# Kernel optimization log

Hardware: AMD Instinct MI355X
Metric: run time of the kernel (lower is better)

## Reference

```python
import jax, jax.numpy as jnp
import numpy as np

B, T, D, H, L, C = 64, 256, 128, 1024, 5, 10


def setup_inputs() -> dict:
    key = jax.random.key(0)
    ks = jax.random.split(key, 6)
    def init(k, shape, fan_in):
        return jax.random.normal(k, shape, jnp.float32) / np.float32(np.sqrt(fan_in))
    x = jax.random.normal(ks[0], (B, T, D), jnp.float32)
    Wx0 = init(ks[1], (D, 4 * H), D)            # layer 0 input weights
    Wxs = init(ks[2], (L - 1, H, 4 * H), H)     # layers 1..L-1 input weights
    Whs = init(ks[3], (L, H, 4 * H), H)         # recurrent weights
    bs = jnp.zeros((L, 4 * H), jnp.float32)     # gate biases
    W_head = init(ks[4], (H, C), H)
    b_head = jnp.zeros((C,), jnp.float32)
    return {"x": x, "Wx0": Wx0, "Wxs": Wxs, "Whs": Whs, "bs": bs,
            "W_head": W_head, "b_head": b_head}


def _lstm_layer(xs, Wx, Wh, b):
    # xs: [T, B, in_d] time-major; returns hidden sequence [T, B, H]
    Bsz = xs.shape[1]
    Hd = Wh.shape[0]
    def step(carry, x_t):
        c, h = carry
        z = x_t @ Wx + h @ Wh + b            # [B, 4H], gate order i,f,g,o (flax)
        i, f, g, o = jnp.split(z, 4, axis=-1)
        c_new = jax.nn.sigmoid(f) * c + jax.nn.sigmoid(i) * jnp.tanh(g)
        h_new = jax.nn.sigmoid(o) * jnp.tanh(c_new)
        return (c_new, h_new), h_new
    init = (jnp.zeros((Bsz, Hd), xs.dtype), jnp.zeros((Bsz, Hd), xs.dtype))
    _, hs = jax.lax.scan(step, init, xs)
    return hs


def reference(x, Wx0, Wxs, Whs, bs, W_head, b_head):
    xs = jnp.swapaxes(x, 0, 1)                  # [T, B, D]
    xs = _lstm_layer(xs, Wx0, Whs[0], bs[0])
    for l in range(1, L):
        xs = _lstm_layer(xs, Wxs[l - 1], Whs[l], bs[l])
    return xs[-1] @ W_head + b_head             # [B, C] from last timestep
```

## Files before the change

### kernel.cpp

```cpp
#include <hip/hip_runtime.h>
#include <hip/hip_cooperative_groups.h>
#include <hip/hip_bf16.h>
#include <cstddef>

namespace cg = cooperative_groups;

typedef unsigned short u16;
typedef __attribute__((ext_vector_type(8))) short s8;
typedef __attribute__((ext_vector_type(4))) float f4;

constexpr int kB = 64, kT = 256, kD = 128, kH = 1024, kL = 5, kC = 10, kG = 4096;
constexpr int BH = kB * kH;
constexpr size_t WLA_ELEMS = (size_t)256 * 8 * 16384;
constexpr size_t WLB_ELEMS = (size_t)256 * 8 * 2560;
constexpr size_t H_ELEMS = (size_t)kL * 2 * BH;


__device__ __forceinline__ float sigf(float x) { return 1.f / (1.f + __expf(-x)); }
__device__ __forceinline__ float tanh_s(float x) {
  float ax = fabsf(x);
  float e = __expf(-2.f * ax);
  float r = (1.f - e) / (1.f + e);
  return copysignf(r, x);
}
__device__ __forceinline__ void split_bf16(float v, short& hi, short& lo) {
  __hip_bfloat16 h = __float2bfloat16(v);
  hi = __builtin_bit_cast(short, h);
  float fh = __bfloat162float(h);
  __hip_bfloat16 l = __float2bfloat16(v - fh);
  lo = __builtin_bit_cast(short, l);
}
__device__ __forceinline__ short hi_bf16(float v) {
  __hip_bfloat16 h = __float2bfloat16(v);
  return __builtin_bit_cast(short, h);
}
__device__ __forceinline__ float bf2f(u16 v) {
  unsigned u = ((unsigned)v) << 16;
  return __builtin_bit_cast(float, u);
}

__device__ __forceinline__ void dma16(const void* gsrc, void* ldst) {
  __builtin_amdgcn_global_load_lds(
      (const __attribute__((address_space(1))) void*)gsrc,
      (__attribute__((address_space(3))) void*)ldst, 16, 0, 0);
}

__global__ void __launch_bounds__(512) split_wl(const float* __restrict__ Wx0,
                                                const float* __restrict__ Wxs,
                                                const float* __restrict__ Whs,
                                                u16* __restrict__ wlA,
                                                u16* __restrict__ wlB) {
  const int g = blockIdx.x, tid = threadIdx.x;
  const int wv = tid >> 6, lane = tid & 63, quad = lane >> 4, r = lane & 15;
  const int lA = (g >> 6) + 1, jb = g & 63, kq = wv & 3, ch = wv >> 2;
  const float* WxA = Wxs + (size_t)(lA - 1) * kH * kG;
  const float* WhA = Whs + (size_t)lA * kH * kG;

  u16* dA = wlA + (size_t)(g * 8 + wv) * 16384;
  for (int p = 0; p < 16; ++p) {
    int kc = 4 * p + kq;
    const float* W = (kc < 32) ? WxA : WhA;
    int krow0 = (kc & 31) * 32 + quad * 8;
    for (int ntl = 0; ntl < 2; ++ntl) {
      int col = (2 * ch + ntl) * kH + jb * 16 + r;
      s8 l8;
      for (int j = 0; j < 8; ++j) {
        float w = W[(size_t)(krow0 + j) * kG + col];
        short hh, ll;
        split_bf16(w, hh, ll);
        l8[j] = ll;
      }
      *(s8*)(dA + (size_t)((p * 2 + ntl) * 64 + lane) * 8) = l8;
    }
  }

  u16* dB = wlB + (size_t)(g * 8 + wv) * 2560;
  int colB = (r >> 2) * kH + g * 4 + (r & 3);
  for (int j2 = 0; j2 < 4; ++j2) {
    int kb = (wv & 3) + 4 * (2 * j2 + (wv >> 2));
    int krow0 = kb * 32 + quad * 8;
    s8 l8;
    for (int j = 0; j < 8; ++j) {
      float w = Whs[(size_t)(krow0 + j) * kG + colB];
      short hh, ll;
      split_bf16(w, hh, ll);
      l8[j] = ll;
    }
    *(s8*)(dB + (size_t)(j2 * 64 + lane) * 8) = l8;
  }
  {
    int krow0 = (wv & 3) * 32 + quad * 8;
    s8 l8;
    for (int j = 0; j < 8; ++j) {
      float w = Wx0[(size_t)(krow0 + j) * kG + colB];
      short hh, ll;
      split_bf16(w, hh, ll);
      l8[j] = ll;
    }
    *(s8*)(dB + (size_t)(4 * 64 + lane) * 8) = l8;
  }
}

__global__ void __launch_bounds__(512, 2) lstm_persist(
    const float* __restrict__ x, const float* __restrict__ Wx0,
    const float* __restrict__ Wxs, const float* __restrict__ Whs,
    const float* __restrict__ bs, const float* __restrict__ W_head,
    const float* __restrict__ b_head, float* __restrict__ out,
    u16* __restrict__ hhi, u16* __restrict__ hlo,
    const u16* __restrict__ wlA, const u16* __restrict__ wlB) {
  cg::grid_group grid = cg::this_grid();
  __shared__ s8 wpark[8][4][2][64];
  __shared__ s8 wring[8][4][2][64];
  __shared__ float zA[64 * 66];
  __shared__ float zB[64 * 18];

  const int tid = threadIdx.x;
  const int wv = tid >> 6, lane = tid & 63, quad = lane >> 4, r = lane & 15;
  const int ch = wv >> 2, kq = wv & 3;
  const int g = blockIdx.x;
  const int lA = (g >> 6) + 1;
  const int jb = g & 63;
  const int ub = g * 4;

  const float* __restrict__ WxA = Wxs + (size_t)(lA - 1) * kH * kG;
  const float* __restrict__ WhA = Whs + (size_t)lA * kH * kG;

  s8 wA[16][2];
#pragma unroll
  for (int p = 0; p < 16; ++p) {
    int kc = 4 * p + kq;
    const float* W = (kc < 32) ? WxA : WhA;
    int krow0 = (kc & 31) * 32 + quad * 8;
#pragma unroll
    for (int ntl = 0; ntl < 2; ++ntl) {
      int col = (2 * ch + ntl) * kH + jb * 16 + r;
      s8 h8;
#pragma unroll
      for (int j = 0; j < 8; ++j) h8[j] = hi_bf16(W[(size_t)(krow0 + j) * kG + col]);
      wA[p][ntl] = h8;
    }
  }
  s8 wBh[4], wBx;
  {
    int colB = (r >> 2) * kH + ub + (r & 3);
#pragma unroll
    for (int j2 = 0; j2 < 4; ++j2) {
      int kb = (wv & 3) + 4 * (2 * j2 + (wv >> 2));
      int krow0 = kb * 32 + quad * 8;
      s8 h8;
#pragma unroll
      for (int j = 0; j < 8; ++j) h8[j] = hi_bf16(Whs[(size_t)(krow0 + j) * kG + colB]);
      wBh[j2] = h8;
    }
    int krow0 = (wv & 3) * 32 + quad * 8;
    s8 h8;
#pragma unroll
    for (int j = 0; j < 8; ++j) h8[j] = hi_bf16(Wx0[(size_t)(krow0 + j) * kG + colB]);
    wBx = h8;
  }

  const u16* wlAs = wlA + (size_t)(g * 8 + wv) * 16384;
  const u16* wlBs = wlB + (size_t)(g * 8 + wv) * 2560;

#pragma unroll
  for (int p = 0; p < 4; ++p)
#pragma unroll
    for (int ntl = 0; ntl < 2; ++ntl)
      wpark[wv][p][ntl][lane] =
          *(const s8*)(wlAs + (size_t)((p * 2 + ntl) * 64 + lane) * 8);

  float bA[4], bB[4];
  {
    int u = tid & 15;
#pragma unroll
    for (int g4 = 0; g4 < 4; ++g4) bA[g4] = bs[(size_t)lA * kG + g4 * kH + jb * 16 + u];
    int u2 = tid & 3;
#pragma unroll
    for (int g4 = 0; g4 < 4; ++g4) bB[g4] = bs[(size_t)g4 * kH + ub + u2];
  }
  float cA0 = 0.f, cA1 = 0.f, cB0 = 0.f;
  const s8 zf = {0, 0, 0, 0, 0, 0, 0, 0};
  const f4 zero4 = {0.f, 0.f, 0.f, 0.f};
  const int fragbase = kq * 4 + quad;

  __syncthreads();

  for (int s = 0; s < kT + kL - 1; ++s) {
    const int tA = s - lA;
    const int tB = s;

    for (int i = tid; i < 64 * 66; i += 512) zA[i] = 0.f;
    for (int i = tid; i < 64 * 18; i += 512) zB[i] = 0.f;
    __syncthreads();

    if (tA >= 0 && tA < kT) {
      const u16* IH = hhi + (size_t)((lA - 1) * 2 + (tA & 1)) * BH;
      const u16* IL = hlo + (size_t)((lA - 1) * 2 + (tA & 1)) * BH;
      const u16* RH = hhi + (size_t)(lA * 2 + ((tA - 1) & 1)) * BH;
      const u16* RL = hlo + (size_t)(lA * 2 + ((tA - 1) & 1)) * BH;
      const bool zz = (tA == 0);
      f4 accA[2][4];
#pragma unroll
      for (int a = 0; a < 2; ++a)
#pragma unroll
        for (int b = 0; b < 4; ++b) accA[a][b] = zero4;

#pragma unroll
      for (int c = 4; c <= 5; ++c)
#pragma unroll
        for (int ntl = 0; ntl < 2; ++ntl)
          dma16(wlAs + (size_t)((c * 2 + ntl) * 64 + lane) * 8,
                &wring[wv][c & 3][ntl][0]);
      s8 ah_n[4], al_n[4];
#pragma unroll
      for (int mt = 0; mt < 4; ++mt) {
        ah_n[mt] = *(const s8*)(IH + (size_t)(fragbase * 64 + mt * 16 + r) * 8);
        al_n[mt] = *(const s8*)(IL + (size_t)(fragbase * 64 + mt * 16 + r) * 8);
      }

#pragma unroll
      for (int p = 0; p < 16; ++p) {
        const bool curR = (p >= 8);
        __builtin_amdgcn_sched_barrier(0);
        if (p >= 4) {
          asm volatile("s_waitcnt vmcnt(4)" ::: "memory");
          __builtin_amdgcn_sched_barrier(0);
        }
        s8 wl0, wl1;
        if (p < 4) {
          wl0 = wpark[wv][p][0][lane];
          wl1 = wpark[wv][p][1][lane];
        } else {
          wl0 = wring[wv][p & 3][0][lane];
          wl1 = wring[wv][p & 3][1][lane];
        }
        s8 ah_c[4], al_c[4];
#pragma unroll
        for (int mt = 0; mt < 4; ++mt) {
          ah_c[mt] = (curR && zz) ? zf : ah_n[mt];
          al_c[mt] = (curR && zz) ? zf : al_n[mt];
        }
        if (p < 15) {
          const int pn = p + 1;
          const u16* SH = (pn >= 8) ? RH : IH;
          const u16* SL = (pn >= 8) ? RL : IL;
          const int kb8 = ((pn & 7) * 16 + fragbase) * 64;
#pragma unroll
          for (int mt = 0; mt < 4; ++mt) {
            ah_n[mt] = *(const s8*)(SH + (size_t)(kb8 + mt * 16 + r) * 8);
            al_n[mt] = *(const s8*)(SL + (size_t)(kb8 + mt * 16 + r) * 8);
          }
        }
        if (p >= 3 && p <= 12) {
          const int c = p + 3;
#pragma unroll
          for (int ntl = 0; ntl < 2; ++ntl)
            dma16(wlAs + (size_t)((c * 2 + ntl) * 64 + lane) * 8,
                  &wring[wv][c & 3][ntl][0]);
        }
#pragma unroll
        for (int mt = 0; mt < 4; ++mt) {
          f4 a0 = accA[0][mt], a1 = accA[1][mt];
          a0 = __builtin_amdgcn_mfma_f32_16x16x32_bf16(ah_c[mt], wA[p][0], a0, 0, 0, 0);
          a0 = __builtin_amdgcn_mfma_f32_16x16x32_bf16(al_c[mt], wA[p][0], a0, 0, 0, 0);
          a0 = __builtin_amdgcn_mfma_f32_16x16x32_bf16(ah_c[mt], wl0, a0, 0, 0, 0);
          a1 = __builtin_amdgcn_mfma_f32_16x16x32_bf16(ah_c[mt], wA[p][1], a1, 0, 0, 0);
          a1 = __builtin_amdgcn_mfma_f32_16x16x32_bf16(al_c[mt], wA[p][1], a1, 0, 0, 0);
          a1 = __builtin_amdgcn_mfma_f32_16x16x32_bf16(ah_c[mt], wl1, a1, 0, 0, 0);
          accA[0][mt] = a0;
          accA[1][mt] = a1;
        }
      }
#pragma unroll
      for (int ntl = 0; ntl < 2; ++ntl)
#pragma unroll
        for (int mt = 0; mt < 4; ++mt)
#pragma unroll
          for (int v = 0; v < 4; ++v)
            atomicAdd(&zA[(mt * 16 + quad * 4 + v) * 66 + (2 * ch + ntl) * 16 + r],
                      accA[ntl][mt][v]);
    }

    if (tB < kT) {
      const u16* H0H = hhi + (size_t)((tB - 1) & 1) * BH;
      const u16* H0L = hlo + (size_t)((tB - 1) & 1) * BH;
      const bool z0 = (tB == 0);
      f4 accB[4];
#pragma unroll
      for (int b = 0; b < 4; ++b) accB[b] = zero4;

      s8 wlb_n = *(const s8*)(wlBs + (size_t)(0 * 64 + lane) * 8);
      s8 ahb_n[4];
      {
        const int kb0 = (wv & 3) + 4 * (wv >> 2);
        const int kb8 = (kb0 * 4 + quad) * 64;
#pragma unroll
        for (int mt = 0; mt < 4; ++mt)
          ahb_n[mt] = *(const s8*)(H0H + (size_t)(kb8 + mt * 16 + r) * 8);
      }
#pragma unroll
      for (int j2 = 0; j2 < 4; ++j2) {
        const int kb = (wv & 3) + 4 * (2 * j2 + (wv >> 2));
        const int kb8c = (kb * 4 + quad) * 64;
        s8 wlv = wlb_n;
        s8 ahb_c[4];
#pragma unroll
        for (int mt = 0; mt < 4; ++mt) ahb_c[mt] = z0 ? zf : ahb_n[mt];
        if (j2 < 3) {
          wlb_n = *(const s8*)(wlBs + (size_t)((j2 + 1) * 64 + lane) * 8);
          const int kbn = (wv & 3) + 4 * (2 * (j2 + 1) + (wv >> 2));
          const int kb8n = (kbn * 4 + quad) * 64;
#pragma unroll
          for (int mt = 0; mt < 4; ++mt)
            ahb_n[mt] = *(const s8*)(H0H + (size_t)(kb8n + mt * 16 + r) * 8);
        }
        s8 alb[4];
#pragma unroll
        for (int mt = 0; mt < 4; ++mt) {
          s8 v = *(const s8*)(H0L + (size_t)(kb8c + mt * 16 + r) * 8);
          alb[mt] = z0 ? zf : v;
        }
#pragma unroll
        for (int mt = 0; mt < 4; ++mt) {
          f4 a = accB[mt];
          a = __builtin_amdgcn_mfma_f32_16x16x32_bf16(ahb_c[mt], wBh[j2], a, 0, 0, 0);
          a = __builtin_amdgcn_mfma_f32_16x16x32_bf16(alb[mt], wBh[j2], a, 0, 0, 0);
          a = __builtin_amdgcn_mfma_f32_16x16x32_bf16(ahb_c[mt], wlv, a, 0, 0, 0);
          accB[mt] = a;
        }
      }
      if (wv >= 4) {
        const int c = wv - 4;
        s8 wlx = *(const s8*)(wlBs + (size_t)(4 * 64 + lane) * 8);
#pragma unroll
        for (int mt = 0; mt < 4; ++mt) {
          const float* sx =
              x + (size_t)(mt * 16 + r) * kT * kD + (size_t)tB * kD + c * 32 + quad * 8;
          float4 v0 = *(const float4*)sx;
          float4 v1 = *(const float4*)(sx + 4);
          float vv[8] = {v0.x, v0.y, v0.z, v0.w, v1.x, v1.y, v1.z, v1.w};
          s8 xh, xl;
#pragma unroll
          for (int e = 0; e < 8; ++e) {
            short hh, ll;
            split_bf16(vv[e], hh, ll);
            xh[e] = hh;
            xl[e] = ll;
          }
          f4 a = accB[mt];
          a = __builtin_amdgcn_mfma_f32_16x16x32_bf16(xh, wBx, a, 0, 0, 0);
          a = __builtin_amdgcn_mfma_f32_16x16x32_bf16(xl, wBx, a, 0, 0, 0);
          a = __builtin_amdgcn_mfma_f32_16x16x32_bf16(xh, wlx, a, 0, 0, 0);
          accB[mt] = a;
        }
      }
#pragma unroll
      for (int mt = 0; mt < 4; ++mt)
#pragma unroll
        for (int v = 0; v < 4; ++v)
          atomicAdd(&zB[(mt * 16 + quad * 4 + v) * 18 + r], accB[mt][v]);
    }

    __syncthreads();

    if (tA >= 0 && tA < kT) {
      const int par = tA & 1;
      u16* HH = hhi + (size_t)(lA * 2 + par) * BH;
      u16* HL = hlo + (size_t)(lA * 2 + par) * BH;
#pragma unroll
      for (int rp = 0; rp < 2; ++rp) {
        int p2 = tid + 512 * rp;
        int b = p2 >> 4, u = p2 & 15;
        float zi = zA[b * 66 + u] + bA[0];
        float zfg = zA[b * 66 + 16 + u] + bA[1];
        float zg = zA[b * 66 + 32 + u] + bA[2];
        float zo = zA[b * 66 + 48 + u] + bA[3];
        float cp = (tA == 0) ? 0.f : (rp ? cA1 : cA0);
        float cn = sigf(zfg) * cp + sigf(zi) * tanh_s(zg);
        float hn = sigf(zo) * tanh_s(cn);
        if (rp) cA1 = cn; else cA0 = cn;
        short hh, ll;
        split_bf16(hn, hh, ll);
        size_t off = ((size_t)(jb * 2 + (u >> 3)) * 64 + b) * 8 + (u & 7);
        HH[off] = (u16)hh;
        HL[off] = (u16)ll;
      }
    }
    if (tB < kT && tid < 256) {
      const int par = tB & 1;
      u16* HH = hhi + (size_t)par * BH;
      u16* HL = hlo + (size_t)par * BH;
      int b = tid >> 2, u2 = tid & 3;
      float zi = zB[b * 18 + u2] + bB[0];
      float zfg = zB[b * 18 + 4 + u2] + bB[1];
      float zg = zB[b * 18 + 8 + u2] + bB[2];
      float zo = zB[b * 18 + 12 + u2] + bB[3];
      float cp = (tB == 0) ? 0.f : cB0;
      float cn = sigf(zfg) * cp + sigf(zi) * tanh_s(zg);
      float hn = sigf(zo) * tanh_s(cn);
      cB0 = cn;
      short hh, ll;
      split_bf16(hn, hh, ll);
      int uglob = ub + u2;
      size_t off = ((size_t)(uglob >> 3) * 64 + b) * 8 + (uglob & 7);
      HH[off] = (u16)hh;
      HL[off] = (u16)ll;
    }

    grid.sync();
  }

  if (g < 80) {
    int p = g * 8 + wv;
    int b = p / 10, cc = p - b * 10;
    const u16* HH = hhi + (size_t)(4 * 2 + 1) * BH;
    const u16* HL = hlo + (size_t)(4 * 2 + 1) * BH;
    float sum = 0.f;
    for (int j = lane; j < kH; j += 64) {
      size_t off = ((size_t)(j >> 3) * 64 + b) * 8 + (j & 7);
      sum += (bf2f(HH[off]) + bf2f(HL[off])) * W_head[(size_t)j * kC + cc];
    }
#pragma unroll
    for (int off = 32; off > 0; off >>= 1) sum += __shfl_down(sum, off, 64);
    if (lane == 0) out[p] = sum + b_head[cc];
  }
}

static u16* g_wl = nullptr;
__attribute__((constructor)) static void alloc_wl() {
  hipMalloc((void**)&g_wl, (WLA_ELEMS + WLB_ELEMS) * sizeof(u16));
}

extern "C" void kernel_launch(void* const* d_in, const int* in_sizes, int n_in,
                              void* d_out, int out_size, void* d_ws, size_t ws_size,
                              hipStream_t stream) {
  const float* x = (const float*)d_in[0];
  const float* Wx0 = (const float*)d_in[1];
  const float* Wxs = (const float*)d_in[2];
  const float* Whs = (const float*)d_in[3];
  const float* bs = (const float*)d_in[4];
  const float* W_head = (const float*)d_in[5];
  const float* b_head = (const float*)d_in[6];
  float* out = (float*)d_out;

  u16* hhi = (u16*)d_ws;
  u16* hlo = hhi + H_ELEMS;
  u16* ws_wl = hlo + H_ELEMS;
  size_t need = (2 * H_ELEMS + WLA_ELEMS + WLB_ELEMS) * sizeof(u16);
  u16 *wlA, *wlB;
  if (ws_size >= need) {
    wlA = ws_wl;
    wlB = wlA + WLA_ELEMS;
  } else {
    wlA = g_wl;
    wlB = g_wl + WLA_ELEMS;
  }

  split_wl<<<256, 512, 0, stream>>>(Wx0, Wxs, Whs, wlA, wlB);

  void* args[] = {&x, &Wx0, &Wxs, &Whs, &bs, &W_head, &b_head,
                  &out, &hhi, &hlo, &wlA, &wlB};
  hipLaunchCooperativeKernel((void*)lstm_persist, dim3(256), dim3(512), args, 0,
                             stream);
}
```

Before: 25.38 ms.

## Replace cooperative grid.sync with per-step counter barrier and full-history hidden buffers

Replaces the cooperative-groups grid.sync with a custom barrier that uses one atomic counter per step, cleared by the preprocessing kernel, and spin-waits with s_sleep. Hidden states now go to a full-time-history buffer instead of a double-buffered pair, so each step's output slot is written only once and the barrier does not need to reset. New h values are first staged in LDS and then written to global memory as 8-byte atomic stores, which coalesces the writes. The risks are a much larger workspace and reliance on relaxed atomics plus an explicit waitcnt for memory visibility across blocks.

```diff
diff --git a/kernel.cpp b/kernel.cpp
--- a/kernel.cpp
+++ b/kernel.cpp
@@ -3,9 +3,8 @@
 #include <hip/hip_bf16.h>
 #include <cstddef>
 
-namespace cg = cooperative_groups;
-
 typedef unsigned short u16;
+typedef unsigned long long u64t;
 typedef __attribute__((ext_vector_type(8))) short s8;
 typedef __attribute__((ext_vector_type(4))) float f4;
 
@@ -13,7 +12,8 @@
 constexpr int BH = kB * kH;
 constexpr size_t WLA_ELEMS = (size_t)256 * 8 * 16384;
 constexpr size_t WLB_ELEMS = (size_t)256 * 8 * 2560;
-constexpr size_t H_ELEMS = (size_t)kL * 2 * BH;
+constexpr size_t H2_ELEMS = (size_t)kL * kT * BH;
+constexpr int NBLK = 256;
 
 
 __device__ __forceinline__ float sigf(float x) { return 1.f / (1.f + __expf(-x)); }
@@ -39,6 +39,10 @@
   return __builtin_bit_cast(float, u);
 }
 
+__device__ __forceinline__ void sth8(u16* p, u64t v) {
+  __hip_atomic_store((u64t*)p, v, __ATOMIC_RELAXED, __HIP_MEMORY_SCOPE_AGENT);
+}
+
 __device__ __forceinline__ void dma16(const void* gsrc, void* ldst) {
   __builtin_amdgcn_global_load_lds(
       (const __attribute__((address_space(1))) void*)gsrc,
@@ -49,12 +53,15 @@
                                                 const float* __restrict__ Wxs,
                                                 const float* __restrict__ Whs,
                                                 u16* __restrict__ wlA,
-                                                u16* __restrict__ wlB) {
+                                                u16* __restrict__ wlB,
+                                                unsigned* __restrict__ bar) {
   const int g = blockIdx.x, tid = threadIdx.x;
   const int wv = tid >> 6, lane = tid & 63, quad = lane >> 4, r = lane & 15;
   const int lA = (g >> 6) + 1, jb = g & 63, kq = wv & 3, ch = wv >> 2;
   const float* WxA = Wxs + (size_t)(lA - 1) * kH * kG;
   const float* WhA = Whs + (size_t)lA * kH * kG;
+
+  if (g == 0 && tid < 512) bar[tid] = 0;
 
   u16* dA = wlA + (size_t)(g * 8 + wv) * 16384;
   for (int p = 0; p < 16; ++p) {
@@ -107,12 +114,14 @@
     const float* __restrict__ bs, const float* __restrict__ W_head,
     const float* __restrict__ b_head, float* __restrict__ out,
     u16* __restrict__ hhi, u16* __restrict__ hlo,
-    const u16* __restrict__ wlA, const u16* __restrict__ wlB) {
-  cg::grid_group grid = cg::this_grid();
+    const u16* __restrict__ wlA, const u16* __restrict__ wlB,
+    unsigned* __restrict__ bar) {
   __shared__ s8 wpark[8][4][2][64];
   __shared__ s8 wring[8][4][2][64];
   __shared__ float zA[64 * 66];
   __shared__ float zB[64 * 18];
+  __shared__ u16 hstA[2][128][8];
+  __shared__ u16 hstB[2][64][4];
 
   const int tid = threadIdx.x;
   const int wv = tid >> 6, lane = tid & 63, quad = lane >> 4, r = lane & 15;
@@ -194,10 +203,11 @@
     __syncthreads();
 
     if (tA >= 0 && tA < kT) {
-      const u16* IH = hhi + (size_t)((lA - 1) * 2 + (tA & 1)) * BH;
-      const u16* IL = hlo + (size_t)((lA - 1) * 2 + (tA & 1)) * BH;
-      const u16* RH = hhi + (size_t)(lA * 2 + ((tA - 1) & 1)) * BH;
-      const u16* RL = hlo + (size_t)(lA * 2 + ((tA - 1) & 1)) * BH;
+      const int tAm1 = (tA > 0) ? tA - 1 : 0;
+      const u16* IH = hhi + ((size_t)(lA - 1) * kT + tA) * BH;
+      const u16* IL = hlo + ((size_t)(lA - 1) * kT + tA) * BH;
+      const u16* RH = hhi + ((size_t)lA * kT + tAm1) * BH;
+      const u16* RL = hlo + ((size_t)lA * kT + tAm1) * BH;
       const bool zz = (tA == 0);
       f4 accA[2][4];
 #pragma unroll
@@ -282,8 +292,9 @@
     }
 
     if (tB < kT) {
-      const u16* H0H = hhi + (size_t)((tB - 1) & 1) * BH;
-      const u16* H0L = hlo + (size_t)((tB - 1) & 1) * BH;
+      const int tBm1 = (tB > 0) ? tB - 1 : 0;
+      const u16* H0H = hhi + (size_t)tBm1 * BH;
+      const u16* H0L = hlo + (size_t)tBm1 * BH;
       const bool z0 = (tB == 0);
       f4 accB[4];
 #pragma unroll
@@ -364,9 +375,6 @@
     __syncthreads();
 
     if (tA >= 0 && tA < kT) {
-      const int par = tA & 1;
-      u16* HH = hhi + (size_t)(lA * 2 + par) * BH;
-      u16* HL = hlo + (size_t)(lA * 2 + par) * BH;
 #pragma unroll
       for (int rp = 0; rp < 2; ++rp) {
         int p2 = tid + 512 * rp;
@@ -381,15 +389,11 @@
         if (rp) cA1 = cn; else cA0 = cn;
         short hh, ll;
         split_bf16(hn, hh, ll);
-        size_t off = ((size_t)(jb * 2 + (u >> 3)) * 64 + b) * 8 + (u & 7);
-        HH[off] = (u16)hh;
-        HL[off] = (u16)ll;
+        hstA[0][(u >> 3) * 64 + b][u & 7] = (u16)hh;
+        hstA[1][(u >> 3) * 64 + b][u & 7] = (u16)ll;
       }
     }
     if (tB < kT && tid < 256) {
-      const int par = tB & 1;
-      u16* HH = hhi + (size_t)par * BH;
-      u16* HL = hlo + (size_t)par * BH;
       int b = tid >> 2, u2 = tid & 3;
       float zi = zB[b * 18 + u2] + bB[0];
       float zfg = zB[b * 18 + 4 + u2] + bB[1];
@@ -401,20 +405,42 @@
       cB0 = cn;
       short hh, ll;
       split_bf16(hn, hh, ll);
-      int uglob = ub + u2;
-      size_t off = ((size_t)(uglob >> 3) * 64 + b) * 8 + (uglob & 7);
-      HH[off] = (u16)hh;
-      HL[off] = (u16)ll;
-    }
-
-    grid.sync();
+      hstB[0][b][u2] = (u16)hh;
+      hstB[1][b][u2] = (u16)ll;
+    }
+    __syncthreads();
+
+    if (tA >= 0 && tA < kT) {
+      u16* HA = ((wv < 4) ? hhi : hlo) + ((size_t)lA * kT + tA) * BH;
+      const int arr = wv >> 2;
+      const int ci = (wv & 3) * 64 + lane;
+      const int gi = ci >> 1, half = ci & 1;
+      u64t v = *(const u64t*)&hstA[arr][gi][half * 4];
+      sth8(HA + ((size_t)(jb * 2 + (gi >> 6)) * 64 + (gi & 63)) * 8 + half * 4, v);
+    }
+    if (tB < kT && wv < 2) {
+      u16* HB = (wv ? hlo : hhi) + (size_t)tB * BH;
+      u64t v = *(const u64t*)&hstB[wv][lane][0];
+      sth8(HB + ((size_t)(ub >> 3) * 64 + lane) * 8 + (ub & 7), v);
+    }
+
+    asm volatile("s_waitcnt vmcnt(0) lgkmcnt(0)" ::: "memory");
+    __syncthreads();
+    if (tid == 0) {
+      __hip_atomic_fetch_add(&bar[s], 1u, __ATOMIC_RELAXED, __HIP_MEMORY_SCOPE_AGENT);
+      while (__hip_atomic_load(&bar[s], __ATOMIC_RELAXED, __HIP_MEMORY_SCOPE_AGENT) <
+             (unsigned)NBLK)
+        __builtin_amdgcn_s_sleep(1);
+    }
+    __syncthreads();
+    asm volatile("" ::: "memory");
   }
 
   if (g < 80) {
     int p = g * 8 + wv;
     int b = p / 10, cc = p - b * 10;
-    const u16* HH = hhi + (size_t)(4 * 2 + 1) * BH;
-    const u16* HL = hlo + (size_t)(4 * 2 + 1) * BH;
+    const u16* HH = hhi + ((size_t)kL * kT - 1) * BH;
+    const u16* HL = hlo + ((size_t)kL * kT - 1) * BH;
     float sum = 0.f;
     for (int j = lane; j < kH; j += 64) {
       size_t off = ((size_t)(j >> 3) * 64 + b) * 8 + (j & 7);
@@ -428,7 +454,8 @@
 
 static u16* g_wl = nullptr;
 __attribute__((constructor)) static void alloc_wl() {
-  hipMalloc((void**)&g_wl, (WLA_ELEMS + WLB_ELEMS) * sizeof(u16));
+  hipMalloc((void**)&g_wl,
+            (WLA_ELEMS + WLB_ELEMS + 2 * H2_ELEMS) * sizeof(u16) + 4096);
 }
 
 extern "C" void kernel_launch(void* const* d_in, const int* in_sizes, int n_in,
@@ -443,23 +470,18 @@
   const float* b_head = (const float*)d_in[6];
   float* out = (float*)d_out;
 
-  u16* hhi = (u16*)d_ws;
-  u16* hlo = hhi + H_ELEMS;
-  u16* ws_wl = hlo + H_ELEMS;
-  size_t need = (2 * H_ELEMS + WLA_ELEMS + WLB_ELEMS) * sizeof(u16);
-  u16 *wlA, *wlB;
-  if (ws_size >= need) {
-    wlA = ws_wl;
-    wlB = wlA + WLA_ELEMS;
-  } else {
-    wlA = g_wl;
-    wlB = g_wl + WLA_ELEMS;
-  }
-
-  split_wl<<<256, 512, 0, stream>>>(Wx0, Wxs, Whs, wlA, wlB);
+  size_t need = (2 * H2_ELEMS + WLA_ELEMS + WLB_ELEMS) * sizeof(u16) + 4096;
+  u16* base = (ws_size >= need) ? (u16*)d_ws : g_wl;
+  u16* hhi = base;
+  u16* hlo = hhi + H2_ELEMS;
+  u16* wlA = hlo + H2_ELEMS;
+  u16* wlB = wlA + WLA_ELEMS;
+  unsigned* bar = (unsigned*)(wlB + WLB_ELEMS);
+
+  split_wl<<<256, 512, 0, stream>>>(Wx0, Wxs, Whs, wlA, wlB, bar);
 
   void* args[] = {&x, &Wx0, &Wxs, &Whs, &bs, &W_head, &b_head,
-                  &out, &hhi, &hlo, &wlA, &wlB};
+                  &out, &hhi, &hlo, &wlA, &wlB, &bar};
   hipLaunchCooperativeKernel((void*)lstm_persist, dim3(256), dim3(512), args, 0,
                              stream);
 }
```

New measurement: 20.58 ms. 18.9% less time.
